# Optimization experiments

Hardware: AMD Instinct MI355X
Metric: run time of the kernel (lower is better)

Reference implementation:

```python
import jax, jax.numpy as jnp
import numpy as np

B, E, S, H = 4, 1024, 2048, 16  # batch, dim, seq_len, n_heads


def setup_inputs() -> dict:
    key = jax.random.key(0)
    ks = jax.random.split(key, 7)
    x = jax.random.normal(ks[0], (B, E, S), dtype=jnp.float32)
    in_w = jax.random.normal(ks[1], (E, E), dtype=jnp.float32) * (1.0 / np.sqrt(E))
    in_b = jnp.zeros((E,), dtype=jnp.float32)
    out_w = jax.random.normal(ks[2], (E, E), dtype=jnp.float32) * (1.0 / np.sqrt(E))
    out_b = jnp.zeros((E,), dtype=jnp.float32)
    mix_w = jax.random.normal(ks[3], (H, S), dtype=jnp.float32)
    mix_b = jnp.zeros((H, S), dtype=jnp.float32)
    return {"x": x, "in_w": in_w, "in_b": in_b, "out_w": out_w,
            "out_b": out_b, "mix_w": mix_w, "mix_b": mix_b}


def _head_matrices(mix_w):
    # First H/2 heads: column-repeat causal M[i,j] = v[j] if j >= i else 0.
    # Last  H/2 heads: row-repeat causal    M[i,j] = v[i] if j >= i else 0.
    idx = jnp.arange(S)
    mask = idx[None, :] >= idx[:, None]  # (S, S), True where j >= i
    Wcol = jnp.where(mask[None], mix_w[: H // 2, None, :], jnp.zeros((), mix_w.dtype))
    Wrow = jnp.where(mask[None], mix_w[H // 2 :, :, None], jnp.zeros((), mix_w.dtype))
    return jnp.concatenate([Wcol, Wrow], axis=0)  # (H, S, S)


def reference(x, in_w, in_b, out_w, out_b, mix_w, mix_b):
    e = E // H  # per-head channel dim
    xt = jnp.transpose(x, (0, 2, 1))           # b t e
    xt = xt @ in_w.T + in_b                    # in_proj
    # 'b t (h e) -> b h e t'
    p = jnp.transpose(xt.reshape(B, S, H, e), (0, 2, 3, 1))
    Wm = _head_matrices(mix_w)                 # (H, S, S)
    # bmm per (batch, head): (e, S) @ (S, S)
    out = jnp.einsum('bhet,hts->bhes', p, Wm) + mix_b[None, :, None, :]
    # 'b h e t -> b t (h e)'
    out = jnp.transpose(out, (0, 3, 1, 2)).reshape(B, S, E)
    out = out @ out_w.T + out_b                # out_proj
    return jnp.transpose(out, (0, 2, 1))       # b e t
```

## Files before the change

### kernel.cpp

```cpp
#include <hip/hip_runtime.h>

#define B_ 4
#define E_ 1024
#define S_ 2048
#define H_ 16
#define K_ 1024

#define NCH 32
#define CS  (S_/NCH)

typedef __bf16 bf16x8 __attribute__((ext_vector_type(8)));
typedef float  f32x4  __attribute__((ext_vector_type(4)));

__device__ __forceinline__ unsigned short f2bf(float f) {
  unsigned u = __float_as_uint(f);
  u += 0x7fffu + ((u >> 16) & 1u);
  return (unsigned short)(u >> 16);
}
__device__ __forceinline__ float bf2f(unsigned short h) {
  return __uint_as_float(((unsigned)h) << 16);
}

__global__ __launch_bounds__(256)
void convert_weights(const float* __restrict__ a, const float* __restrict__ c,
                     unsigned short* __restrict__ wa, unsigned short* __restrict__ wb)
{
  const int per = (E_ * E_) / 4;
  int i = blockIdx.x * 256 + threadIdx.x;
  const float4* src = (i < per) ? (const float4*)a : (const float4*)c;
  unsigned short* dst = (i < per) ? wa : wb;
  int j = (i < per) ? i : i - per;
  float4 v = src[j];
  ushort4 o;
  o.x = f2bf(v.x); o.y = f2bf(v.y); o.z = f2bf(v.z); o.w = f2bf(v.w);
  *(ushort4*)(dst + (long)j * 4) = o;
}

__global__ __launch_bounds__(256)
void transpose_convert(const float* __restrict__ x, unsigned short* __restrict__ xt)
{
  __shared__ float t[64][65];
  const int b  = blockIdx.z;
  const int e0 = blockIdx.y * 64;
  const int s0 = blockIdx.x * 64;
  const int tx = threadIdx.x & 63, ty = threadIdx.x >> 6;

  const float* xp = x + ((long)b * E_ + e0) * S_ + s0;
#pragma unroll
  for (int r = 0; r < 16; ++r) {
    int row = r * 4 + ty;
    t[row][tx] = xp[(long)row * S_ + tx];
  }
  __syncthreads();
  unsigned short* xo = xt + ((long)b * S_ + s0) * E_ + e0;
#pragma unroll
  for (int p = 0; p < 2; ++p) {
    int s = p * 32 + (threadIdx.x >> 3);
    int e = (threadIdx.x & 7) * 8;
    unsigned short v[8];
#pragma unroll
    for (int j = 0; j < 8; ++j) v[j] = f2bf(t[e + j][s]);
    *(ushort4*)(xo + (long)s * E_ + e)     = make_ushort4(v[0], v[1], v[2], v[3]);
    *(ushort4*)(xo + (long)s * E_ + e + 4) = make_ushort4(v[4], v[5], v[6], v[7]);
  }
}

#define BB1 49152

__device__ __forceinline__ void stage_a(char* smem, const unsigned short* __restrict__ Ab,
                                        int bb, int t, int ks, int tid, int wid) {
#pragma unroll
  for (int j = 0; j < 2; ++j) {
    int chunk = j * 512 + tid;
    int row = chunk >> 2;
    int cb  = (chunk & 3) << 4;
    int cbs = cb ^ (((row >> 1) & 3) << 4);
    const unsigned short* src = Ab + (long)row * K_ + t * 64 + ks * 32 + (cbs >> 1);
    __builtin_amdgcn_global_load_lds(
        (const __attribute__((address_space(1))) void*)src,
        (__attribute__((address_space(3))) void*)(smem + bb + ks * 16384 + j * 8192 + wid * 1024),
        16, 0, 0);
  }
}

__device__ __forceinline__ void stage_b(char* smem, const unsigned short* __restrict__ Bb,
                                        int bb, int t, int ks, int tid, int wid) {
  int row = tid >> 2;
  int cb  = (tid & 3) << 4;
  int cbs = cb ^ (((row >> 1) & 3) << 4);
  const unsigned short* src = Bb + (long)row * K_ + t * 64 + ks * 32 + (cbs >> 1);
  __builtin_amdgcn_global_load_lds(
      (const __attribute__((address_space(1))) void*)src,
      (__attribute__((address_space(3))) void*)(smem + bb + 32768 + ks * 8192 + wid * 1024),
      16, 0, 0);
}

template<int MH>
__device__ __forceinline__ void phase_reads(const char* smem, int bb, int ks,
    int wm, int wn, int lr, int lg, bf16x8 af[4], bf16x8 bfr[2]) {
#pragma unroll
  for (int q = 0; q < 4; ++q) {
    int row = wm * 128 + (MH * 4 + q) * 16 + lr;
    int cb  = (lg * 16) ^ (((row >> 1) & 3) << 4);
    af[q] = *(const bf16x8*)(smem + bb + ks * 16384 + row * 64 + cb);
  }
  if (MH == 0) {
#pragma unroll
    for (int q = 0; q < 2; ++q) {
      int row = wn * 32 + q * 16 + lr;
      int cb  = (lg * 16) ^ (((row >> 1) & 3) << 4);
      bfr[q] = *(const bf16x8*)(smem + bb + 32768 + ks * 8192 + row * 64 + cb);
    }
  }
}

template<int MH>
__device__ __forceinline__ void phase_mfma(const bf16x8 af[4], const bf16x8 bfr[2],
                                           f32x4 acc[8][2]) {
  __builtin_amdgcn_s_setprio(1);
#pragma unroll
  for (int q = 0; q < 4; ++q)
#pragma unroll
    for (int nf = 0; nf < 2; ++nf)
      acc[MH * 4 + q][nf] = __builtin_amdgcn_mfma_f32_16x16x32_bf16(
          af[q], bfr[nf], acc[MH * 4 + q][nf], 0, 0, 0);
  __builtin_amdgcn_s_setprio(0);
}

#define FENCE asm volatile("" ::: "memory")
#define BAR do { FENCE; __builtin_amdgcn_s_barrier(); FENCE; } while (0)
#define VM(n) asm volatile("s_waitcnt vmcnt(" #n ")" ::: "memory")
#define NOWAIT (void)0

#define PH(bb, ks, mh, STAGE, WAIT) do {                        \
    bf16x8 af[4];                                               \
    phase_reads<mh>(smem, bb, ks, wm, wn, lr, lg, af, bfr);     \
    STAGE;                                                      \
    WAIT;                                                       \
    BAR;                                                        \
    asm volatile("s_waitcnt lgkmcnt(0)" ::: "memory");          \
    phase_mfma<mh>(af, bfr, acc);                               \
    BAR;                                                        \
  } while (0)

template<int VARIANT>
__global__ __launch_bounds__(512, 2)
void gemm8p(const unsigned short* __restrict__ A, const unsigned short* __restrict__ Bw,
            void* __restrict__ Cout, const float* __restrict__ bias)
{
  extern __shared__ char smem[];
  const int tid  = threadIdx.x;
  const int lane = tid & 63, wid = tid >> 6;
  const int wm = wid >> 2, wn = wid & 3;
  const int lr = lane & 15, lg = lane >> 4;

  const int bid = blockIdx.x;
  const int xcd = bid & 7;
  const int j8  = bid >> 3;
  const int tm  = (xcd << 2) | (j8 & 3);
  const int tn  = j8 >> 2;

  const unsigned short* Ab = A  + (long)tm * 256 * K_;
  const unsigned short* Bb = Bw + (long)tn * 128 * K_;

  f32x4 acc[8][2] = {};
  bf16x8 bfr[2];

  stage_a(smem, Ab, 0, 0, 0, tid, wid);
  stage_b(smem, Bb, 0, 0, 0, tid, wid);
  stage_a(smem, Ab, 0, 0, 1, tid, wid);
  stage_b(smem, Bb, 0, 0, 1, tid, wid);
  stage_a(smem, Ab, BB1, 1, 0, tid, wid);
  stage_b(smem, Bb, BB1, 1, 0, tid, wid);
  VM(6);
  BAR;

  for (int i = 0; i < 7; ++i) {
    const int t1 = 2 * i + 1, t2 = 2 * i + 2, t3 = 2 * i + 3;
    PH(0,   0, 0, stage_a(smem, Ab, BB1, t1, 1, tid, wid), NOWAIT);
    PH(0,   0, 1, stage_b(smem, Bb, BB1, t1, 1, tid, wid), VM(6));
    PH(0,   1, 0, stage_a(smem, Ab, 0,   t2, 0, tid, wid), NOWAIT);
    PH(0,   1, 1, stage_b(smem, Bb, 0,   t2, 0, tid, wid), VM(6));
    PH(BB1, 0, 0, stage_a(smem, Ab, 0,   t2, 1, tid, wid), NOWAIT);
    PH(BB1, 0, 1, stage_b(smem, Bb, 0,   t2, 1, tid, wid), VM(6));
    PH(BB1, 1, 0, stage_a(smem, Ab, BB1, t3, 0, tid, wid), NOWAIT);
    PH(BB1, 1, 1, stage_b(smem, Bb, BB1, t3, 0, tid, wid), VM(6));
  }
  PH(0,   0, 0, stage_a(smem, Ab, BB1, 15, 1, tid, wid), NOWAIT);
  PH(0,   0, 1, stage_b(smem, Bb, BB1, 15, 1, tid, wid), VM(6));
  PH(0,   1, 0, NOWAIT, NOWAIT);
  PH(0,   1, 1, NOWAIT, VM(3));
  PH(BB1, 0, 0, NOWAIT, NOWAIT);
  PH(BB1, 0, 1, NOWAIT, VM(0));
  PH(BB1, 1, 0, NOWAIT, NOWAIT);
  PH(BB1, 1, 1, NOWAIT, NOWAIT);

#pragma unroll
  for (int nf = 0; nf < 2; ++nf) {
    const int c = tn * 128 + wn * 32 + nf * 16 + lr;
    const float bv = bias[c];
#pragma unroll
    for (int mf = 0; mf < 8; ++mf) {
      const int r0 = tm * 256 + wm * 128 + mf * 16 + lg * 4;
      if constexpr (VARIANT == 0) {
#pragma unroll
        for (int j = 0; j < 4; ++j)
          ((unsigned short*)Cout)[(long)(r0 + j) * E_ + c] = f2bf(acc[mf][nf][j] + bv);
      } else {
        const int s = r0 & (S_ - 1);
        const int b = r0 >> 11;
        float4 v;
        v.x = acc[mf][nf][0] + bv; v.y = acc[mf][nf][1] + bv;
        v.z = acc[mf][nf][2] + bv; v.w = acc[mf][nf][3] + bv;
        *(float4*)((float*)Cout + ((long)b * E_ + c) * S_ + s) = v;
      }
    }
  }
}

__global__ __launch_bounds__(256)
void scan_part(const unsigned short* __restrict__ yt, const float* __restrict__ mixw,
               float* __restrict__ part)
{
  const int b  = blockIdx.z;
  const int c  = blockIdx.y * 256 + threadIdx.x;
  const int ch = blockIdx.x;
  const int h  = c >> 6;
  const unsigned short* yp = yt + ((long)b * S_ + ch * CS) * E_ + c;
  float sum = 0.f;
  if (h < 8) {
#pragma unroll 4
    for (int s = 0; s < CS; ++s) sum += bf2f(yp[(long)s * E_]);
  } else {
    const float* mw = mixw + (long)h * S_ + ch * CS;
#pragma unroll 4
    for (int s = 0; s < CS; ++s) sum += bf2f(yp[(long)s * E_]) * mw[s];
  }
  part[((long)b * NCH + ch) * E_ + c] = sum;
}

__global__ __launch_bounds__(256)
void scan_final(const unsigned short* __restrict__ yt, const float* __restrict__ mixw,
                const float* __restrict__ mixb, const float* __restrict__ part,
                unsigned short* __restrict__ zt)
{
  const int b  = blockIdx.z;
  const int c  = blockIdx.y * 256 + threadIdx.x;
  const int ch = blockIdx.x;
  const int h  = c >> 6;
  float acc = 0.f;
  for (int p = 0; p < ch; ++p) acc += part[((long)b * NCH + p) * E_ + c];
  const unsigned short* yp = yt + ((long)b * S_ + ch * CS) * E_ + c;
  unsigned short*       zp = zt + ((long)b * S_ + ch * CS) * E_ + c;
  const float* mw = mixw + (long)h * S_ + ch * CS;
  const float* mb = mixb + (long)h * S_ + ch * CS;
  if (h < 8) {
    for (int s = 0; s < CS; ++s) {
      acc += bf2f(yp[(long)s * E_]);
      zp[(long)s * E_] = f2bf(fmaf(acc, mw[s], mb[s]));
    }
  } else {
    for (int s = 0; s < CS; ++s) {
      acc += bf2f(yp[(long)s * E_]) * mw[s];
      zp[(long)s * E_] = f2bf(acc + mb[s]);
    }
  }
}

extern "C" void kernel_launch(void* const* d_in, const int* in_sizes, int n_in,
                              void* d_out, int out_size, void* d_ws, size_t ws_size,
                              hipStream_t stream)
{
  (void)in_sizes; (void)n_in; (void)out_size; (void)ws_size;
  const float* x     = (const float*)d_in[0];
  const float* in_w  = (const float*)d_in[1];
  const float* in_b  = (const float*)d_in[2];
  const float* out_w = (const float*)d_in[3];
  const float* out_b = (const float*)d_in[4];
  const float* mix_w = (const float*)d_in[5];
  const float* mix_b = (const float*)d_in[6];

  char* ws = (char*)d_ws;
  unsigned short* Xt  = (unsigned short*)(ws);
  unsigned short* Yt  = (unsigned short*)(ws + (size_t)16 * 1024 * 1024);
  unsigned short* W1b = (unsigned short*)(ws + (size_t)32 * 1024 * 1024);
  unsigned short* W2b = (unsigned short*)(ws + (size_t)34 * 1024 * 1024);
  float*          part = (float*)(ws + (size_t)36 * 1024 * 1024);
  unsigned short* Zt  = Xt;

  hipFuncSetAttribute((const void*)gemm8p<0>, hipFuncAttributeMaxDynamicSharedMemorySize, 98304);
  hipFuncSetAttribute((const void*)gemm8p<1>, hipFuncAttributeMaxDynamicSharedMemorySize, 98304);

  convert_weights<<<dim3((2 * E_ * E_ / 4) / 256), 256, 0, stream>>>(in_w, out_w, W1b, W2b);

  transpose_convert<<<dim3(S_ / 64, E_ / 64, B_), 256, 0, stream>>>(x, Xt);

  gemm8p<0><<<dim3(256), 512, 98304, stream>>>(Xt, W1b, Yt, in_b);

  scan_part<<<dim3(NCH, E_ / 256, B_), 256, 0, stream>>>(Yt, mix_w, part);
  scan_final<<<dim3(NCH, E_ / 256, B_), 256, 0, stream>>>(Yt, mix_w, mix_b, part, Zt);

  gemm8p<1><<<dim3(256), 512, 98304, stream>>>(Zt, W2b, d_out, out_b);
}
```

Before: 85.25 us.

## Fuse scan partial sums into GEMM epilogue, merge weight conversion into transpose

Computes the per-chunk scan partial sums directly in the first GEMM's epilogue using warp shuffles, which removes the separate scan_part kernel and its re-read of Yt. Weight conversion is folded into the transpose kernel as an extra grid z-slice, dropping one launch. The GEMM main loop goes from 8 half-phases to 4 larger phases that each load all 8 A fragments and issue 16 MFMAs per barrier pair. In exchange, register pressure goes up, and the epilogue now does scattered mix_w loads and shuffles.

```diff
diff --git a/kernel.cpp b/kernel.cpp
--- a/kernel.cpp
+++ b/kernel.cpp
@@ -22,23 +22,27 @@
 }
 
 __global__ __launch_bounds__(256)
-void convert_weights(const float* __restrict__ a, const float* __restrict__ c,
-                     unsigned short* __restrict__ wa, unsigned short* __restrict__ wb)
-{
-  const int per = (E_ * E_) / 4;
-  int i = blockIdx.x * 256 + threadIdx.x;
-  const float4* src = (i < per) ? (const float4*)a : (const float4*)c;
-  unsigned short* dst = (i < per) ? wa : wb;
-  int j = (i < per) ? i : i - per;
-  float4 v = src[j];
-  ushort4 o;
-  o.x = f2bf(v.x); o.y = f2bf(v.y); o.z = f2bf(v.z); o.w = f2bf(v.w);
-  *(ushort4*)(dst + (long)j * 4) = o;
-}
-
-__global__ __launch_bounds__(256)
-void transpose_convert(const float* __restrict__ x, unsigned short* __restrict__ xt)
-{
+void tc_kernel(const float* __restrict__ x, unsigned short* __restrict__ xt,
+               const float* __restrict__ inw, const float* __restrict__ outw,
+               unsigned short* __restrict__ w1, unsigned short* __restrict__ w2)
+{
+  if (blockIdx.z == 4) {
+    const int per = (E_ * E_) / 4;
+    const int fid = blockIdx.y * 32 + blockIdx.x;
+#pragma unroll
+    for (int k = 0; k < 4; ++k) {
+      int i = fid * 1024 + k * 256 + threadIdx.x;
+      const float4* src = (i < per) ? (const float4*)inw : (const float4*)outw;
+      unsigned short* dst = (i < per) ? w1 : w2;
+      int j = (i < per) ? i : i - per;
+      float4 v = src[j];
+      ushort4 o;
+      o.x = f2bf(v.x); o.y = f2bf(v.y); o.z = f2bf(v.z); o.w = f2bf(v.w);
+      *(ushort4*)(dst + (long)j * 4) = o;
+    }
+    return;
+  }
+
   __shared__ float t[64][65];
   const int b  = blockIdx.z;
   const int e0 = blockIdx.y * 64;
@@ -95,58 +99,45 @@
       16, 0, 0);
 }
 
-template<int MH>
-__device__ __forceinline__ void phase_reads(const char* smem, int bb, int ks,
-    int wm, int wn, int lr, int lg, bf16x8 af[4], bf16x8 bfr[2]) {
-#pragma unroll
-  for (int q = 0; q < 4; ++q) {
-    int row = wm * 128 + (MH * 4 + q) * 16 + lr;
-    int cb  = (lg * 16) ^ (((row >> 1) & 3) << 4);
-    af[q] = *(const bf16x8*)(smem + bb + ks * 16384 + row * 64 + cb);
-  }
-  if (MH == 0) {
-#pragma unroll
-    for (int q = 0; q < 2; ++q) {
-      int row = wn * 32 + q * 16 + lr;
-      int cb  = (lg * 16) ^ (((row >> 1) & 3) << 4);
-      bfr[q] = *(const bf16x8*)(smem + bb + 32768 + ks * 8192 + row * 64 + cb);
-    }
-  }
-}
-
-template<int MH>
-__device__ __forceinline__ void phase_mfma(const bf16x8 af[4], const bf16x8 bfr[2],
-                                           f32x4 acc[8][2]) {
-  __builtin_amdgcn_s_setprio(1);
-#pragma unroll
-  for (int q = 0; q < 4; ++q)
-#pragma unroll
-    for (int nf = 0; nf < 2; ++nf)
-      acc[MH * 4 + q][nf] = __builtin_amdgcn_mfma_f32_16x16x32_bf16(
-          af[q], bfr[nf], acc[MH * 4 + q][nf], 0, 0, 0);
-  __builtin_amdgcn_s_setprio(0);
-}
-
 #define FENCE asm volatile("" ::: "memory")
 #define BAR do { FENCE; __builtin_amdgcn_s_barrier(); FENCE; } while (0)
 #define VM(n) asm volatile("s_waitcnt vmcnt(" #n ")" ::: "memory")
 #define NOWAIT (void)0
 
-#define PH(bb, ks, mh, STAGE, WAIT) do {                        \
-    bf16x8 af[4];                                               \
-    phase_reads<mh>(smem, bb, ks, wm, wn, lr, lg, af, bfr);     \
-    STAGE;                                                      \
-    WAIT;                                                       \
-    BAR;                                                        \
-    asm volatile("s_waitcnt lgkmcnt(0)" ::: "memory");          \
-    phase_mfma<mh>(af, bfr, acc);                               \
-    BAR;                                                        \
+#define PH(bb, ks, STAGE, WAIT) do {                                        \
+    bf16x8 af[8], bfv[2];                                                   \
+    _Pragma("unroll")                                                       \
+    for (int q = 0; q < 8; ++q) {                                           \
+      int row = wm * 128 + q * 16 + lr;                                     \
+      int cb = (lg * 16) ^ (((row >> 1) & 3) << 4);                         \
+      af[q] = *(const bf16x8*)(smem + (bb) + (ks) * 16384 + row * 64 + cb); \
+    }                                                                       \
+    _Pragma("unroll")                                                       \
+    for (int q = 0; q < 2; ++q) {                                           \
+      int row = wn * 32 + q * 16 + lr;                                      \
+      int cb = (lg * 16) ^ (((row >> 1) & 3) << 4);                         \
+      bfv[q] = *(const bf16x8*)(smem + (bb) + 32768 + (ks) * 8192 + row * 64 + cb); \
+    }                                                                       \
+    STAGE;                                                                  \
+    WAIT;                                                                   \
+    BAR;                                                                    \
+    asm volatile("s_waitcnt lgkmcnt(0)" ::: "memory");                      \
+    __builtin_amdgcn_s_setprio(1);                                          \
+    _Pragma("unroll")                                                       \
+    for (int q = 0; q < 8; ++q)                                             \
+      _Pragma("unroll")                                                     \
+      for (int nf = 0; nf < 2; ++nf)                                        \
+        acc[q][nf] = __builtin_amdgcn_mfma_f32_16x16x32_bf16(               \
+            af[q], bfv[nf], acc[q][nf], 0, 0, 0);                           \
+    __builtin_amdgcn_s_setprio(0);                                          \
+    BAR;                                                                    \
   } while (0)
 
 template<int VARIANT>
 __global__ __launch_bounds__(512, 2)
-void gemm8p(const unsigned short* __restrict__ A, const unsigned short* __restrict__ Bw,
-            void* __restrict__ Cout, const float* __restrict__ bias)
+void gemm4p(const unsigned short* __restrict__ A, const unsigned short* __restrict__ Bw,
+            void* __restrict__ Cout, const float* __restrict__ bias,
+            const float* __restrict__ mixw, float* __restrict__ part)
 {
   extern __shared__ char smem[];
   const int tid  = threadIdx.x;
@@ -164,49 +155,58 @@
   const unsigned short* Bb = Bw + (long)tn * 128 * K_;
 
   f32x4 acc[8][2] = {};
-  bf16x8 bfr[2];
-
-  stage_a(smem, Ab, 0, 0, 0, tid, wid);
-  stage_b(smem, Bb, 0, 0, 0, tid, wid);
-  stage_a(smem, Ab, 0, 0, 1, tid, wid);
-  stage_b(smem, Bb, 0, 0, 1, tid, wid);
-  stage_a(smem, Ab, BB1, 1, 0, tid, wid);
-  stage_b(smem, Bb, BB1, 1, 0, tid, wid);
+
+  stage_a(smem, Ab, 0,   0, 0, tid, wid);  stage_b(smem, Bb, 0,   0, 0, tid, wid);
+  stage_a(smem, Ab, 0,   0, 1, tid, wid);  stage_b(smem, Bb, 0,   0, 1, tid, wid);
+  stage_a(smem, Ab, BB1, 1, 0, tid, wid);  stage_b(smem, Bb, BB1, 1, 0, tid, wid);
   VM(6);
   BAR;
 
-  for (int i = 0; i < 7; ++i) {
-    const int t1 = 2 * i + 1, t2 = 2 * i + 2, t3 = 2 * i + 3;
-    PH(0,   0, 0, stage_a(smem, Ab, BB1, t1, 1, tid, wid), NOWAIT);
-    PH(0,   0, 1, stage_b(smem, Bb, BB1, t1, 1, tid, wid), VM(6));
-    PH(0,   1, 0, stage_a(smem, Ab, 0,   t2, 0, tid, wid), NOWAIT);
-    PH(0,   1, 1, stage_b(smem, Bb, 0,   t2, 0, tid, wid), VM(6));
-    PH(BB1, 0, 0, stage_a(smem, Ab, 0,   t2, 1, tid, wid), NOWAIT);
-    PH(BB1, 0, 1, stage_b(smem, Bb, 0,   t2, 1, tid, wid), VM(6));
-    PH(BB1, 1, 0, stage_a(smem, Ab, BB1, t3, 0, tid, wid), NOWAIT);
-    PH(BB1, 1, 1, stage_b(smem, Bb, BB1, t3, 0, tid, wid), VM(6));
-  }
-  PH(0,   0, 0, stage_a(smem, Ab, BB1, 15, 1, tid, wid), NOWAIT);
-  PH(0,   0, 1, stage_b(smem, Bb, BB1, 15, 1, tid, wid), VM(6));
-  PH(0,   1, 0, NOWAIT, NOWAIT);
-  PH(0,   1, 1, NOWAIT, VM(3));
-  PH(BB1, 0, 0, NOWAIT, NOWAIT);
-  PH(BB1, 0, 1, NOWAIT, VM(0));
-  PH(BB1, 1, 0, NOWAIT, NOWAIT);
-  PH(BB1, 1, 1, NOWAIT, NOWAIT);
+  for (int t = 0; t < 14; ++t) {
+    const int bb = (t & 1) ? BB1 : 0;
+    const int nb = (t & 1) ? 0 : BB1;
+    PH(bb, 0, { stage_a(smem, Ab, nb, t + 1, 1, tid, wid);
+                stage_b(smem, Bb, nb, t + 1, 1, tid, wid); }, VM(6));
+    PH(bb, 1, { stage_a(smem, Ab, bb, t + 2, 0, tid, wid);
+                stage_b(smem, Bb, bb, t + 2, 0, tid, wid); }, VM(6));
+  }
+  PH(0, 0, { stage_a(smem, Ab, BB1, 15, 1, tid, wid);
+             stage_b(smem, Bb, BB1, 15, 1, tid, wid); }, VM(6));
+  PH(0,   1, NOWAIT, VM(3));
+  PH(BB1, 0, NOWAIT, VM(0));
+  PH(BB1, 1, NOWAIT, NOWAIT);
 
 #pragma unroll
   for (int nf = 0; nf < 2; ++nf) {
     const int c = tn * 128 + wn * 32 + nf * 16 + lr;
     const float bv = bias[c];
-#pragma unroll
-    for (int mf = 0; mf < 8; ++mf) {
-      const int r0 = tm * 256 + wm * 128 + mf * 16 + lg * 4;
-      if constexpr (VARIANT == 0) {
-#pragma unroll
-        for (int j = 0; j < 4; ++j)
-          ((unsigned short*)Cout)[(long)(r0 + j) * E_ + c] = f2bf(acc[mf][nf][j] + bv);
-      } else {
+    if constexpr (VARIANT == 0) {
+      const int h  = c >> 6;
+      const int bt = tm >> 3;
+      const int sb = ((tm & 7) << 8) + wm * 128;
+      float sm0 = 0.f, sm1 = 0.f;
+#pragma unroll
+      for (int mf = 0; mf < 8; ++mf) {
+#pragma unroll
+        for (int j = 0; j < 4; ++j) {
+          const int sl = sb + mf * 16 + lg * 4 + j;
+          float v = acc[mf][nf][j] + bv;
+          ((unsigned short*)Cout)[((long)bt * S_ + sl) * E_ + c] = f2bf(v);
+          float w = (h < 8) ? v : v * mixw[h * S_ + sl];
+          if (mf < 4) sm0 += w; else sm1 += w;
+        }
+      }
+      sm0 += __shfl_xor(sm0, 16, 64);  sm0 += __shfl_xor(sm0, 32, 64);
+      sm1 += __shfl_xor(sm1, 16, 64);  sm1 += __shfl_xor(sm1, 32, 64);
+      if (lg == 0) {
+        const int ch0 = ((tm & 7) << 2) + wm * 2;
+        part[((long)bt * NCH + ch0)     * E_ + c] = sm0;
+        part[((long)bt * NCH + ch0 + 1) * E_ + c] = sm1;
+      }
+    } else {
+#pragma unroll
+      for (int mf = 0; mf < 8; ++mf) {
+        const int r0 = tm * 256 + wm * 128 + mf * 16 + lg * 4;
         const int s = r0 & (S_ - 1);
         const int b = r0 >> 11;
         float4 v;
@@ -216,27 +216,6 @@
       }
     }
   }
-}
-
-__global__ __launch_bounds__(256)
-void scan_part(const unsigned short* __restrict__ yt, const float* __restrict__ mixw,
-               float* __restrict__ part)
-{
-  const int b  = blockIdx.z;
-  const int c  = blockIdx.y * 256 + threadIdx.x;
-  const int ch = blockIdx.x;
-  const int h  = c >> 6;
-  const unsigned short* yp = yt + ((long)b * S_ + ch * CS) * E_ + c;
-  float sum = 0.f;
-  if (h < 8) {
-#pragma unroll 4
-    for (int s = 0; s < CS; ++s) sum += bf2f(yp[(long)s * E_]);
-  } else {
-    const float* mw = mixw + (long)h * S_ + ch * CS;
-#pragma unroll 4
-    for (int s = 0; s < CS; ++s) sum += bf2f(yp[(long)s * E_]) * mw[s];
-  }
-  part[((long)b * NCH + ch) * E_ + c] = sum;
 }
 
 __global__ __launch_bounds__(256)
@@ -288,17 +267,14 @@
   float*          part = (float*)(ws + (size_t)36 * 1024 * 1024);
   unsigned short* Zt  = Xt;
 
-  hipFuncSetAttribute((const void*)gemm8p<0>, hipFuncAttributeMaxDynamicSharedMemorySize, 98304);
-  hipFuncSetAttribute((const void*)gemm8p<1>, hipFuncAttributeMaxDynamicSharedMemorySize, 98304);
-
-  convert_weights<<<dim3((2 * E_ * E_ / 4) / 256), 256, 0, stream>>>(in_w, out_w, W1b, W2b);
-
-  transpose_convert<<<dim3(S_ / 64, E_ / 64, B_), 256, 0, stream>>>(x, Xt);
-
-  gemm8p<0><<<dim3(256), 512, 98304, stream>>>(Xt, W1b, Yt, in_b);
-
-  scan_part<<<dim3(NCH, E_ / 256, B_), 256, 0, stream>>>(Yt, mix_w, part);
+  hipFuncSetAttribute((const void*)gemm4p<0>, hipFuncAttributeMaxDynamicSharedMemorySize, 98304);
+  hipFuncSetAttribute((const void*)gemm4p<1>, hipFuncAttributeMaxDynamicSharedMemorySize, 98304);
+
+  tc_kernel<<<dim3(S_ / 64, E_ / 64, 5), 256, 0, stream>>>(x, Xt, in_w, out_w, W1b, W2b);
+
+  gemm4p<0><<<dim3(256), 512, 98304, stream>>>(Xt, W1b, Yt, in_b, mix_w, part);
+
   scan_final<<<dim3(NCH, E_ / 256, B_), 256, 0, stream>>>(Yt, mix_w, mix_b, part, Zt);
 
-  gemm8p<1><<<dim3(256), 512, 98304, stream>>>(Zt, W2b, d_out, out_b);
-}
+  gemm4p<1><<<dim3(256), 512, 98304, stream>>>(Zt, W2b, d_out, out_b, nullptr, nullptr);
+}
```

New measurement: 85.39 us. Within noise of the previous version (+0.2%).
